# Optimization experiments

Hardware: AMD Instinct MI355X
Metric: run time of the kernel (lower is better)

## Reference

```python
import jax, jax.numpy as jnp
import numpy as np

EMBED_DIM = 256
NUM_HEADS = 8
HEAD_DIM = EMBED_DIM // NUM_HEADS
SCALE = HEAD_DIM ** -0.5  # note: scale uses head_dim even though attention is over full D
EPS = 1e-12  # torch F.normalize eps


def setup_inputs() -> dict:
    key = jax.random.key(0)
    k1, k2, k3 = jax.random.split(key, 3)
    B, Nq, Nk, D = 4, 4096, 4096, EMBED_DIM
    return {
        "query": jax.random.normal(k1, (B, Nq, D), dtype=jnp.float32),
        "key": jax.random.normal(k2, (B, Nk, D), dtype=jnp.float32),
        "value": jax.random.normal(k3, (B, Nk, D), dtype=jnp.float32),
    }


def _l2_normalize(x):
    # matches torch.nn.functional.normalize(x, dim=-1): x / max(||x||, eps)
    n = jnp.linalg.norm(x, axis=-1, keepdims=True)
    return x / jnp.maximum(n, EPS)


def reference(query, key, value):
    q = _l2_normalize(query)          # (B, Nq, D)
    k = _l2_normalize(key)            # (B, Nk, D)
    scores = jnp.einsum("bqd,bkd->bqk", q, k) * SCALE  # (B, Nq, Nk) cosine sims
    attn = jax.nn.softmax(scores, axis=-1)
    return jnp.einsum("bqk,bkd->bqd", attn, value)     # (B, Nq, D)
```

## Files before the change

### kernel.cpp

```cpp
#include <hip/hip_runtime.h>


#define NQ 4096
#define DIM 256
#define NROWS 16384
#define BM 64
#define BN 64
#define KSPLIT 4
#define NITER 16
#define PSTRIDE 68

typedef __attribute__((ext_vector_type(8))) short bf16x8;
typedef __attribute__((ext_vector_type(4))) float f32x4;
typedef __attribute__((ext_vector_type(16))) float f32x16;

__device__ __forceinline__ unsigned short f2bf(float f) {
  unsigned int u = __float_as_uint(f);
  u += 0x7fffu + ((u >> 16) & 1u);
  return (unsigned short)(u >> 16);
}

__device__ __forceinline__ float bf2f(unsigned short h) {
  return __uint_as_float((unsigned int)h << 16);
}

__device__ __forceinline__ unsigned int pack2bf(float a, float b) {
  unsigned int ua = __float_as_uint(a) + 0x8000u;
  unsigned int ub = __float_as_uint(b) + 0x8000u;
  return __builtin_amdgcn_perm(ub, ua, 0x07060302u);
}

__device__ __forceinline__ void gload16(const void* g, void* l) {
  __builtin_amdgcn_global_load_lds(
      (const __attribute__((address_space(1))) unsigned int*)g,
      (__attribute__((address_space(3))) unsigned int*)l, 16, 0, 0);
}

__global__ __launch_bounds__(256) void prep(
    const float* __restrict__ Q, const float* __restrict__ K,
    const float* __restrict__ V,
    unsigned short* __restrict__ Qrm, unsigned short* __restrict__ Kfm,
    unsigned short* __restrict__ Vfm)
{
  __shared__ unsigned short vt[64 * 264];
  const int blk = blockIdx.x, tid = threadIdx.x;
  const int wave = tid >> 6, lane = tid & 63;
  if (blk < 4096) {
    const int R = blk * 4 + wave;
    float4 v = *(const float4*)(Q + (size_t)R * DIM + lane * 4);
    float ss = v.x*v.x + v.y*v.y + v.z*v.z + v.w*v.w;
    #pragma unroll
    for (int off = 1; off < 64; off <<= 1) ss += __shfl_xor(ss, off, 64);
    float scale = (0.17677669529663687f * 1.4426950408889634f)
                  / fmaxf(sqrtf(ss), 1e-12f);
    ushort4 o;
    o.x = f2bf(v.x*scale); o.y = f2bf(v.y*scale);
    o.z = f2bf(v.z*scale); o.w = f2bf(v.w*scale);
    *(ushort4*)(Qrm + (size_t)R * DIM + lane * 4) = o;
  } else if (blk < 4352) {
    const int kt = blk - 4096;
    #pragma unroll
    for (int i = 0; i < 16; i++) {
      const int n = i*4 + wave;
      float4 v = *(const float4*)(K + ((size_t)kt*64 + n) * DIM + lane * 4);
      float ss = v.x*v.x + v.y*v.y + v.z*v.z + v.w*v.w;
      #pragma unroll
      for (int off = 1; off < 64; off <<= 1) ss += __shfl_xor(ss, off, 64);
      float scale = 1.0f / fmaxf(sqrtf(ss), 1e-12f);
      ushort4 o;
      o.x = f2bf(v.x*scale); o.y = f2bf(v.y*scale);
      o.z = f2bf(v.z*scale); o.w = f2bf(v.w*scale);
      *(ushort4*)(vt + n*264 + lane*4) = o;
    }
    __syncthreads();
    #pragma unroll
    for (int s = 0; s < 8; s++) {
      const int ch = tid + 256*s;
      const int c = ch >> 6, n = ch & 63;
      bf16x8 val = *(const bf16x8*)(vt + n*264 + c*8);
      *(bf16x8*)(Kfm + (size_t)kt*16384 + (size_t)ch*8) = val;
    }
  } else {
    const int NS = blk - 4352;
    #pragma unroll
    for (int i = 0; i < 4; i++) {
      const int e = tid + 256*i;
      const int nl = e >> 6, d = (e & 63) * 4;
      float4 v = *(const float4*)(V + ((size_t)NS*16 + nl)*DIM + d);
      ushort4 o;
      o.x = f2bf(v.x); o.y = f2bf(v.y); o.z = f2bf(v.z); o.w = f2bf(v.w);
      *(ushort4*)(vt + nl*264 + d) = o;
    }
    __syncthreads();
    #pragma unroll
    for (int i = 0; i < 2; i++) {
      const int ch = tid + 256*i;
      const int db = ch >> 6, ln = ch & 63;
      const int row0 = (ln >> 5) * 8, dd = db*32 + (ln & 31);
      ushort4 a, b;
      a.x = vt[(row0+0)*264 + dd]; a.y = vt[(row0+1)*264 + dd];
      a.z = vt[(row0+2)*264 + dd]; a.w = vt[(row0+3)*264 + dd];
      b.x = vt[(row0+4)*264 + dd]; b.y = vt[(row0+5)*264 + dd];
      b.z = vt[(row0+6)*264 + dd]; b.w = vt[(row0+7)*264 + dd];
      size_t base = ((size_t)(NS*8 + db)*64 + ln)*8;
      *(ushort4*)(Vfm + base)     = a;
      *(ushort4*)(Vfm + base + 4) = b;
    }
  }
}

__global__ __launch_bounds__(256, 4) void attn(
    const unsigned short* __restrict__ Qrm,
    const unsigned short* __restrict__ Kfm,
    const unsigned short* __restrict__ Vfm,
    unsigned short* __restrict__ Opart, float* __restrict__ lpart)
{
  __shared__ unsigned short Klds[32 * 64 * 8];
  __shared__ unsigned short Plds[BM * PSTRIDE];

  const int tid = threadIdx.x, wave = tid >> 6, lane = tid & 63;
  const int l15 = lane & 15, l4 = lane >> 4;
  const int blk = blockIdx.x;
  const int g = blk & 15, qt = blk >> 4;
  const int b = g >> 2, ks = g & 3;
  const int Rq0 = b*NQ + qt*BM;
  const int n0base = b*NQ + ks*(NQ/KSPLIT);
  const int mi = wave & 1, ni = wave >> 1;

  bf16x8 qf[2][8];
  #pragma unroll
  for (int mt = 0; mt < 2; mt++) {
    const unsigned short* qrow = Qrm + (size_t)(Rq0 + mi*32 + mt*16 + l15) * DIM + l4*8;
    #pragma unroll
    for (int kg = 0; kg < 8; kg++)
      qf[mt][kg] = *(const bf16x8*)(qrow + kg*32);
  }

  f32x16 oacc[2][2] = {};
  float lacc[2] = {};

  auto stage = [&](int kt) {
    const unsigned short* src = Kfm + (size_t)((n0base + kt*BN) >> 6) * (32*64*8);
    #pragma unroll
    for (int jj = 0; jj < 4; jj++) {
      const int c = wave*8 + jj*2;
      gload16(src + (size_t)c*512 + lane*8,     Klds + (size_t)c*512);
      gload16(src + (size_t)(c+1)*512 + lane*8, Klds + (size_t)(c+1)*512);
    }
  };

  stage(0);

  for (int kt = 0; kt < NITER; kt++) {
    __syncthreads();

    f32x4 sacc[2][2] = {};
    #pragma unroll
    for (int kg = 0; kg < 8; kg++) {
      bf16x8 kf[2];
      #pragma unroll
      for (int nt = 0; nt < 2; nt++) {
        const int nrow = ni*32 + nt*16 + l15;
        const int c = kg*4 + l4;
        kf[nt] = *(const bf16x8*)(Klds + ((size_t)(c*64 + nrow))*8);
      }
      #pragma unroll
      for (int nt = 0; nt < 2; nt++)
        #pragma unroll
        for (int mt = 0; mt < 2; mt++)
          sacc[nt][mt] = __builtin_amdgcn_mfma_f32_16x16x32_bf16(
              kf[nt], qf[mt][kg], sacc[nt][mt], 0, 0, 0);
    }

    #pragma unroll
    for (int nt = 0; nt < 2; nt++)
      #pragma unroll
      for (int mt = 0; mt < 2; mt++) {
        float p0 = __builtin_amdgcn_exp2f(sacc[nt][mt][0]);
        float p1 = __builtin_amdgcn_exp2f(sacc[nt][mt][1]);
        float p2 = __builtin_amdgcn_exp2f(sacc[nt][mt][2]);
        float p3 = __builtin_amdgcn_exp2f(sacc[nt][mt][3]);
        lacc[mt] += (p0 + p1) + (p2 + p3);
        uint2 pk;
        pk.x = pack2bf(p0, p1);
        pk.y = pack2bf(p2, p3);
        const int m = mi*32 + mt*16 + l15;
        const int n = ni*32 + nt*16 + 4*l4;
        *(uint2*)(Plds + m*PSTRIDE + n) = pk;
      }

    __syncthreads();

    if (kt + 1 < NITER) stage(kt + 1);

    const int NB0 = (n0base + kt*BN) >> 4;
    #pragma unroll
    for (int kstep = 0; kstep < 4; kstep++) {
      bf16x8 pf[2], vf[2];
      #pragma unroll
      for (int mt2 = 0; mt2 < 2; mt2++)
        pf[mt2] = *(const bf16x8*)(Plds + (mt2*32 + (lane & 31))*PSTRIDE
                                   + kstep*16 + 8*(lane >> 5));
      #pragma unroll
      for (int dt = 0; dt < 2; dt++) {
        const int db = wave*2 + dt;
        vf[dt] = *(const bf16x8*)(Vfm + ((size_t)((NB0 + kstep)*8 + db)*64 + lane)*8);
      }
      #pragma unroll
      for (int mt2 = 0; mt2 < 2; mt2++)
        #pragma unroll
        for (int dt = 0; dt < 2; dt++)
          oacc[mt2][dt] = __builtin_amdgcn_mfma_f32_32x32x16_bf16(
              pf[mt2], vf[dt], oacc[mt2][dt], 0, 0, 0);
    }
  }

  #pragma unroll
  for (int mt = 0; mt < 2; mt++) {
    float s = lacc[mt];
    s += __shfl_xor(s, 16, 64);
    s += __shfl_xor(s, 32, 64);
    if (l4 == 0)
      lpart[(size_t)(ks*2 + ni)*NROWS + Rq0 + mi*32 + mt*16 + l15] = s;
  }

  #pragma unroll
  for (int mt2 = 0; mt2 < 2; mt2++)
    #pragma unroll
    for (int dt = 0; dt < 2; dt++)
      #pragma unroll
      for (int reg = 0; reg < 16; reg++) {
        const int m = mt2*32 + 4*(lane >> 5) + (reg & 3) + 8*(reg >> 2);
        const int d = wave*64 + dt*32 + (lane & 31);
        Opart[((size_t)(ks*NROWS + Rq0 + m))*DIM + d] = f2bf(oacc[mt2][dt][reg]);
      }
}

__global__ __launch_bounds__(256) void combine(
    const unsigned short* __restrict__ Opart, const float* __restrict__ lpart,
    float* __restrict__ out)
{
  const size_t idx = (size_t)blockIdx.x*256 + threadIdx.x;
  const size_t e = idx*4;
  const int R = (int)(e >> 8);
  float acc[4] = {0.f, 0.f, 0.f, 0.f};
  #pragma unroll
  for (int s = 0; s < 4; s++) {
    ushort4 o = *(const ushort4*)(Opart + (size_t)s*NROWS*DIM + e);
    acc[0] += bf2f(o.x); acc[1] += bf2f(o.y);
    acc[2] += bf2f(o.z); acc[3] += bf2f(o.w);
  }
  float ls = 0.f;
  #pragma unroll
  for (int s = 0; s < 8; s++) ls += lpart[(size_t)s*NROWS + R];
  float inv = 1.0f / ls;
  float4 o;
  o.x = acc[0]*inv; o.y = acc[1]*inv; o.z = acc[2]*inv; o.w = acc[3]*inv;
  *(float4*)(out + e) = o;
}

extern "C" void kernel_launch(void* const* d_in, const int* in_sizes, int n_in,
                              void* d_out, int out_size, void* d_ws, size_t ws_size,
                              hipStream_t stream) {
  const float* Q = (const float*)d_in[0];
  const float* K = (const float*)d_in[1];
  const float* V = (const float*)d_in[2];
  char* ws = (char*)d_ws;
  unsigned short* Qrm  = (unsigned short*)(ws);
  unsigned short* Kfm  = (unsigned short*)(ws + 8388608);
  unsigned short* Vfm  = (unsigned short*)(ws + 16777216);
  unsigned short* Opart = (unsigned short*)(ws + 25165824);
  float* lpart = (float*)(ws + 58720256);

  prep<<<5376, 256, 0, stream>>>(Q, K, V, Qrm, Kfm, Vfm);
  attn<<<1024, 256, 0, stream>>>(Qrm, Kfm, Vfm, Opart, lpart);
  combine<<<4096, 256, 0, stream>>>(Opart, lpart, (float*)d_out);
}
```

Before: 196.3 us.

## Fuse Q normalization into attention and halve the key split

Q normalization moves out of the prep kernel and into the attention kernel, which reads fp32 Q directly, normalizes and converts it into LDS, then loads its fragments from there. This removes the Qrm round trip through global memory. The key-split factor drops from 4 to 2 with twice the iterations per block, which cuts the partial-output traffic written by attention and read by combine. Prep now handles K in 32-row halves. In exchange only 512 attention blocks launch, with launch bounds lowered to 2 blocks per CU, so the GPU may be less fully occupied. Combine still sums 4 lpart slices, which depends on how the hidden attention code writes lpart (likely 2 per split).

```diff
diff --git a/kernel.cpp b/kernel.cpp
--- a/kernel.cpp
+++ b/kernel.cpp
@@ -6,8 +6,8 @@
 #define NROWS 16384
 #define BM 64
 #define BN 64
-#define KSPLIT 4
-#define NITER 16
+#define KSPLIT 2
+#define NITER 32
 #define PSTRIDE 68
 
 typedef __attribute__((ext_vector_type(8))) short bf16x8;
@@ -37,32 +37,19 @@
 }
 
 __global__ __launch_bounds__(256) void prep(
-    const float* __restrict__ Q, const float* __restrict__ K,
-    const float* __restrict__ V,
-    unsigned short* __restrict__ Qrm, unsigned short* __restrict__ Kfm,
-    unsigned short* __restrict__ Vfm)
+    const float* __restrict__ K, const float* __restrict__ V,
+    unsigned short* __restrict__ Kfm, unsigned short* __restrict__ Vfm)
 {
-  __shared__ unsigned short vt[64 * 264];
+  __shared__ unsigned short vt[32 * 264];
   const int blk = blockIdx.x, tid = threadIdx.x;
   const int wave = tid >> 6, lane = tid & 63;
-  if (blk < 4096) {
-    const int R = blk * 4 + wave;
-    float4 v = *(const float4*)(Q + (size_t)R * DIM + lane * 4);
-    float ss = v.x*v.x + v.y*v.y + v.z*v.z + v.w*v.w;
-    #pragma unroll
-    for (int off = 1; off < 64; off <<= 1) ss += __shfl_xor(ss, off, 64);
-    float scale = (0.17677669529663687f * 1.4426950408889634f)
-                  / fmaxf(sqrtf(ss), 1e-12f);
-    ushort4 o;
-    o.x = f2bf(v.x*scale); o.y = f2bf(v.y*scale);
-    o.z = f2bf(v.z*scale); o.w = f2bf(v.w*scale);
-    *(ushort4*)(Qrm + (size_t)R * DIM + lane * 4) = o;
-  } else if (blk < 4352) {
-    const int kt = blk - 4096;
-    #pragma unroll
-    for (int i = 0; i < 16; i++) {
-      const int n = i*4 + wave;
-      float4 v = *(const float4*)(K + ((size_t)kt*64 + n) * DIM + lane * 4);
+  if (blk < 512) {
+    const int kt2 = blk;
+    const int kt = kt2 >> 1, h = kt2 & 1;
+    #pragma unroll
+    for (int i = 0; i < 8; i++) {
+      const int r = wave*8 + i;
+      float4 v = *(const float4*)(K + ((size_t)kt2*32 + r) * DIM + lane * 4);
       float ss = v.x*v.x + v.y*v.y + v.z*v.z + v.w*v.w;
       #pragma unroll
       for (int off = 1; off < 64; off <<= 1) ss += __shfl_xor(ss, off, 64);
@@ -70,18 +57,19 @@
       ushort4 o;
       o.x = f2bf(v.x*scale); o.y = f2bf(v.y*scale);
       o.z = f2bf(v.z*scale); o.w = f2bf(v.w*scale);
-      *(ushort4*)(vt + n*264 + lane*4) = o;
-    }
-    __syncthreads();
-    #pragma unroll
-    for (int s = 0; s < 8; s++) {
+      *(ushort4*)(vt + r*264 + lane*4) = o;
+    }
+    __syncthreads();
+    #pragma unroll
+    for (int s = 0; s < 4; s++) {
       const int ch = tid + 256*s;
-      const int c = ch >> 6, n = ch & 63;
-      bf16x8 val = *(const bf16x8*)(vt + n*264 + c*8);
-      *(bf16x8*)(Kfm + (size_t)kt*16384 + (size_t)ch*8) = val;
+      const int c = ch >> 5, r = ch & 31;
+      const int n = h*32 + r;
+      bf16x8 val = *(const bf16x8*)(vt + r*264 + c*8);
+      *(bf16x8*)(Kfm + (size_t)kt*16384 + (size_t)(c*64 + n)*8) = val;
     }
   } else {
-    const int NS = blk - 4352;
+    const int NS = blk - 512;
     #pragma unroll
     for (int i = 0; i < 4; i++) {
       const int e = tid + 256*i;
@@ -109,8 +97,8 @@
   }
 }
 
-__global__ __launch_bounds__(256, 4) void attn(
-    const unsigned short* __restrict__ Qrm,
+__global__ __launch_bounds__(256, 2) void attn(
+    const float* __restrict__ Qg,
     const unsigned short* __restrict__ Kfm,
     const unsigned short* __restrict__ Vfm,
     unsigned short* __restrict__ Opart, float* __restrict__ lpart)
@@ -121,20 +109,40 @@
   const int tid = threadIdx.x, wave = tid >> 6, lane = tid & 63;
   const int l15 = lane & 15, l4 = lane >> 4;
   const int blk = blockIdx.x;
-  const int g = blk & 15, qt = blk >> 4;
-  const int b = g >> 2, ks = g & 3;
+  const int g = blk & 7, qt = blk >> 3;
+  const int b = g >> 1, ks = g & 1;
   const int Rq0 = b*NQ + qt*BM;
   const int n0base = b*NQ + ks*(NQ/KSPLIT);
   const int mi = wave & 1, ni = wave >> 1;
 
+  {
+    unsigned short* Qlds = Klds;
+    #pragma unroll
+    for (int i = 0; i < 16; i++) {
+      const int r = wave*16 + i;
+      float4 v = *(const float4*)(Qg + (size_t)(Rq0 + r)*DIM + lane*4);
+      float ss = v.x*v.x + v.y*v.y + v.z*v.z + v.w*v.w;
+      #pragma unroll
+      for (int off = 1; off < 64; off <<= 1) ss += __shfl_xor(ss, off, 64);
+      float scale = (0.17677669529663687f * 1.4426950408889634f)
+                    / fmaxf(sqrtf(ss), 1e-12f);
+      ushort4 o;
+      o.x = f2bf(v.x*scale); o.y = f2bf(v.y*scale);
+      o.z = f2bf(v.z*scale); o.w = f2bf(v.w*scale);
+      *(ushort4*)(Qlds + r*DIM + lane*4) = o;
+    }
+  }
+  __syncthreads();
+
   bf16x8 qf[2][8];
   #pragma unroll
   for (int mt = 0; mt < 2; mt++) {
-    const unsigned short* qrow = Qrm + (size_t)(Rq0 + mi*32 + mt*16 + l15) * DIM + l4*8;
+    const unsigned short* qrow = Klds + (mi*32 + mt*16 + l15)*DIM + l4*8;
     #pragma unroll
     for (int kg = 0; kg < 8; kg++)
       qf[mt][kg] = *(const bf16x8*)(qrow + kg*32);
   }
+  __syncthreads();
 
   f32x16 oacc[2][2] = {};
   float lacc[2] = {};
@@ -243,19 +251,15 @@
   const size_t idx = (size_t)blockIdx.x*256 + threadIdx.x;
   const size_t e = idx*4;
   const int R = (int)(e >> 8);
-  float acc[4] = {0.f, 0.f, 0.f, 0.f};
-  #pragma unroll
-  for (int s = 0; s < 4; s++) {
-    ushort4 o = *(const ushort4*)(Opart + (size_t)s*NROWS*DIM + e);
-    acc[0] += bf2f(o.x); acc[1] += bf2f(o.y);
-    acc[2] += bf2f(o.z); acc[3] += bf2f(o.w);
-  }
-  float ls = 0.f;
-  #pragma unroll
-  for (int s = 0; s < 8; s++) ls += lpart[(size_t)s*NROWS + R];
+  ushort4 o0 = *(const ushort4*)(Opart + e);
+  ushort4 o1 = *(const ushort4*)(Opart + (size_t)NROWS*DIM + e);
+  float ls = lpart[R] + lpart[NROWS + R] + lpart[2*NROWS + R] + lpart[3*NROWS + R];
   float inv = 1.0f / ls;
   float4 o;
-  o.x = acc[0]*inv; o.y = acc[1]*inv; o.z = acc[2]*inv; o.w = acc[3]*inv;
+  o.x = (bf2f(o0.x) + bf2f(o1.x))*inv;
+  o.y = (bf2f(o0.y) + bf2f(o1.y))*inv;
+  o.z = (bf2f(o0.z) + bf2f(o1.z))*inv;
+  o.w = (bf2f(o0.w) + bf2f(o1.w))*inv;
   *(float4*)(out + e) = o;
 }
 
@@ -266,13 +270,12 @@
   const float* K = (const float*)d_in[1];
   const float* V = (const float*)d_in[2];
   char* ws = (char*)d_ws;
-  unsigned short* Qrm  = (unsigned short*)(ws);
-  unsigned short* Kfm  = (unsigned short*)(ws + 8388608);
-  unsigned short* Vfm  = (unsigned short*)(ws + 16777216);
-  unsigned short* Opart = (unsigned short*)(ws + 25165824);
-  float* lpart = (float*)(ws + 58720256);
-
-  prep<<<5376, 256, 0, stream>>>(Q, K, V, Qrm, Kfm, Vfm);
-  attn<<<1024, 256, 0, stream>>>(Qrm, Kfm, Vfm, Opart, lpart);
+  unsigned short* Kfm   = (unsigned short*)(ws);
+  unsigned short* Vfm   = (unsigned short*)(ws + 8388608);
+  unsigned short* Opart = (unsigned short*)(ws + 16777216);
+  float* lpart = (float*)(ws + 33554432);
+
+  prep<<<1536, 256, 0, stream>>>(K, V, Kfm, Vfm);
+  attn<<<512, 256, 0, stream>>>(Q, Kfm, Vfm, Opart, lpart);
   combine<<<4096, 256, 0, stream>>>(Opart, lpart, (float*)d_out);
 }
```

After: 173.5 us. 11.6% less time.

## Quantize normalized Q and K to FP8 and use FP8 MFMA for scores

Applied to the files above, without the earlier changes.

Normalized Q and K are stored as FP8 e4m3 instead of bf16, and the QK^T product uses the fp8 MFMA instruction. The softmax scale moves from the Q prep into a multiply before exp2. The prep kernel is regrouped to handle 16 Q rows per block and half K tiles, which shrinks the workspace and the K staging size in LDS. This halves Q/K bytes and doubles MFMA throughput for the score GEMM, at the cost of reduced score precision. Occupancy hint drops from 4 to 3 blocks per CU.

```diff
diff --git a/kernel.cpp b/kernel.cpp
--- a/kernel.cpp
+++ b/kernel.cpp
@@ -1,4 +1,5 @@
 #include <hip/hip_runtime.h>
+#include <hip/hip_fp8.h>
 
 
 #define NQ 4096
@@ -9,6 +10,7 @@
 #define KSPLIT 4
 #define NITER 16
 #define PSTRIDE 68
+#define SC 0.25508689738717859f
 
 typedef __attribute__((ext_vector_type(8))) short bf16x8;
 typedef __attribute__((ext_vector_type(4))) float f32x4;
@@ -24,6 +26,11 @@
   return __uint_as_float((unsigned int)h << 16);
 }
 
+__device__ __forceinline__ unsigned char f2fp8(float x) {
+  __hip_fp8_e4m3 t(x);
+  return t.__x;
+}
+
 __device__ __forceinline__ unsigned int pack2bf(float a, float b) {
   unsigned int ua = __float_as_uint(a) + 0x8000u;
   unsigned int ub = __float_as_uint(b) + 0x8000u;
@@ -39,49 +46,56 @@
 __global__ __launch_bounds__(256) void prep(
     const float* __restrict__ Q, const float* __restrict__ K,
     const float* __restrict__ V,
-    unsigned short* __restrict__ Qrm, unsigned short* __restrict__ Kfm,
+    unsigned char* __restrict__ Qf8, unsigned char* __restrict__ Kfm,
     unsigned short* __restrict__ Vfm)
 {
-  __shared__ unsigned short vt[64 * 264];
+  __shared__ unsigned short vt[32 * 264];
   const int blk = blockIdx.x, tid = threadIdx.x;
   const int wave = tid >> 6, lane = tid & 63;
-  if (blk < 4096) {
-    const int R = blk * 4 + wave;
-    float4 v = *(const float4*)(Q + (size_t)R * DIM + lane * 4);
-    float ss = v.x*v.x + v.y*v.y + v.z*v.z + v.w*v.w;
-    #pragma unroll
-    for (int off = 1; off < 64; off <<= 1) ss += __shfl_xor(ss, off, 64);
-    float scale = (0.17677669529663687f * 1.4426950408889634f)
-                  / fmaxf(sqrtf(ss), 1e-12f);
-    ushort4 o;
-    o.x = f2bf(v.x*scale); o.y = f2bf(v.y*scale);
-    o.z = f2bf(v.z*scale); o.w = f2bf(v.w*scale);
-    *(ushort4*)(Qrm + (size_t)R * DIM + lane * 4) = o;
-  } else if (blk < 4352) {
-    const int kt = blk - 4096;
-    #pragma unroll
-    for (int i = 0; i < 16; i++) {
-      const int n = i*4 + wave;
-      float4 v = *(const float4*)(K + ((size_t)kt*64 + n) * DIM + lane * 4);
+  if (blk < 1024) {
+    #pragma unroll
+    for (int i = 0; i < 4; i++) {
+      const int R = blk*16 + i*4 + wave;
+      float4 v = *(const float4*)(Q + (size_t)R * DIM + lane * 4);
       float ss = v.x*v.x + v.y*v.y + v.z*v.z + v.w*v.w;
       #pragma unroll
       for (int off = 1; off < 64; off <<= 1) ss += __shfl_xor(ss, off, 64);
-      float scale = 1.0f / fmaxf(sqrtf(ss), 1e-12f);
-      ushort4 o;
-      o.x = f2bf(v.x*scale); o.y = f2bf(v.y*scale);
-      o.z = f2bf(v.z*scale); o.w = f2bf(v.w*scale);
-      *(ushort4*)(vt + n*264 + lane*4) = o;
-    }
-    __syncthreads();
-    #pragma unroll
-    for (int s = 0; s < 8; s++) {
+      float s = 1.0f / fmaxf(sqrtf(ss), 1e-12f);
+      unsigned int pk = (unsigned int)f2fp8(v.x*s)
+                      | ((unsigned int)f2fp8(v.y*s) << 8)
+                      | ((unsigned int)f2fp8(v.z*s) << 16)
+                      | ((unsigned int)f2fp8(v.w*s) << 24);
+      *(unsigned int*)(Qf8 + (size_t)R * DIM + lane * 4) = pk;
+    }
+  } else if (blk < 1536) {
+    const int kt2 = blk - 1024;
+    unsigned char* vtb = (unsigned char*)vt;
+    #pragma unroll
+    for (int i = 0; i < 8; i++) {
+      const int r = wave*8 + i;
+      float4 v = *(const float4*)(K + ((size_t)kt2*32 + r) * DIM + lane * 4);
+      float ss = v.x*v.x + v.y*v.y + v.z*v.z + v.w*v.w;
+      #pragma unroll
+      for (int off = 1; off < 64; off <<= 1) ss += __shfl_xor(ss, off, 64);
+      float s = 1.0f / fmaxf(sqrtf(ss), 1e-12f);
+      unsigned int pk = (unsigned int)f2fp8(v.x*s)
+                      | ((unsigned int)f2fp8(v.y*s) << 8)
+                      | ((unsigned int)f2fp8(v.z*s) << 16)
+                      | ((unsigned int)f2fp8(v.w*s) << 24);
+      *(unsigned int*)(vtb + r*264 + lane*4) = pk;
+    }
+    __syncthreads();
+    const int kt = kt2 >> 1, h = kt2 & 1;
+    #pragma unroll
+    for (int s = 0; s < 4; s++) {
       const int ch = tid + 256*s;
-      const int c = ch >> 6, n = ch & 63;
-      bf16x8 val = *(const bf16x8*)(vt + n*264 + c*8);
-      *(bf16x8*)(Kfm + (size_t)kt*16384 + (size_t)ch*8) = val;
+      const int c = ch >> 5, r = ch & 31;
+      const int n = h*32 + r;
+      long val = *(const long*)(vtb + r*264 + c*8);
+      *(long*)(Kfm + (size_t)kt*16384 + (size_t)(c*64 + n)*8) = val;
     }
   } else {
-    const int NS = blk - 4352;
+    const int NS = blk - 1536;
     #pragma unroll
     for (int i = 0; i < 4; i++) {
       const int e = tid + 256*i;
@@ -109,13 +123,13 @@
   }
 }
 
-__global__ __launch_bounds__(256, 4) void attn(
-    const unsigned short* __restrict__ Qrm,
-    const unsigned short* __restrict__ Kfm,
+__global__ __launch_bounds__(256, 3) void attn(
+    const unsigned char* __restrict__ Qf8,
+    const unsigned char* __restrict__ Kfm,
     const unsigned short* __restrict__ Vfm,
     unsigned short* __restrict__ Opart, float* __restrict__ lpart)
 {
-  __shared__ unsigned short Klds[32 * 64 * 8];
+  __shared__ unsigned char Klds[16384];
   __shared__ unsigned short Plds[BM * PSTRIDE];
 
   const int tid = threadIdx.x, wave = tid >> 6, lane = tid & 63;
@@ -127,25 +141,24 @@
   const int n0base = b*NQ + ks*(NQ/KSPLIT);
   const int mi = wave & 1, ni = wave >> 1;
 
-  bf16x8 qf[2][8];
+  long qf[2][8];
   #pragma unroll
   for (int mt = 0; mt < 2; mt++) {
-    const unsigned short* qrow = Qrm + (size_t)(Rq0 + mi*32 + mt*16 + l15) * DIM + l4*8;
+    const unsigned char* qrow = Qf8 + (size_t)(Rq0 + mi*32 + mt*16 + l15)*DIM + l4*8;
     #pragma unroll
     for (int kg = 0; kg < 8; kg++)
-      qf[mt][kg] = *(const bf16x8*)(qrow + kg*32);
+      qf[mt][kg] = *(const long*)(qrow + kg*32);
   }
 
   f32x16 oacc[2][2] = {};
   float lacc[2] = {};
 
   auto stage = [&](int kt) {
-    const unsigned short* src = Kfm + (size_t)((n0base + kt*BN) >> 6) * (32*64*8);
+    const unsigned char* src = Kfm + (size_t)((n0base + kt*BN) >> 6) * 16384;
     #pragma unroll
     for (int jj = 0; jj < 4; jj++) {
-      const int c = wave*8 + jj*2;
-      gload16(src + (size_t)c*512 + lane*8,     Klds + (size_t)c*512);
-      gload16(src + (size_t)(c+1)*512 + lane*8, Klds + (size_t)(c+1)*512);
+      const int off = wave*4096 + jj*1024 + lane*16;
+      gload16(src + off, Klds + off);
     }
   };
 
@@ -157,18 +170,17 @@
     f32x4 sacc[2][2] = {};
     #pragma unroll
     for (int kg = 0; kg < 8; kg++) {
-      bf16x8 kf[2];
+      long kf[2];
       #pragma unroll
       for (int nt = 0; nt < 2; nt++) {
         const int nrow = ni*32 + nt*16 + l15;
-        const int c = kg*4 + l4;
-        kf[nt] = *(const bf16x8*)(Klds + ((size_t)(c*64 + nrow))*8);
+        kf[nt] = *(const long*)(Klds + (kg*4 + l4)*512 + nrow*8);
       }
       #pragma unroll
       for (int nt = 0; nt < 2; nt++)
         #pragma unroll
         for (int mt = 0; mt < 2; mt++)
-          sacc[nt][mt] = __builtin_amdgcn_mfma_f32_16x16x32_bf16(
+          sacc[nt][mt] = __builtin_amdgcn_mfma_f32_16x16x32_fp8_fp8(
               kf[nt], qf[mt][kg], sacc[nt][mt], 0, 0, 0);
     }
 
@@ -176,10 +188,10 @@
     for (int nt = 0; nt < 2; nt++)
       #pragma unroll
       for (int mt = 0; mt < 2; mt++) {
-        float p0 = __builtin_amdgcn_exp2f(sacc[nt][mt][0]);
-        float p1 = __builtin_amdgcn_exp2f(sacc[nt][mt][1]);
-        float p2 = __builtin_amdgcn_exp2f(sacc[nt][mt][2]);
-        float p3 = __builtin_amdgcn_exp2f(sacc[nt][mt][3]);
+        float p0 = __builtin_amdgcn_exp2f(sacc[nt][mt][0] * SC);
+        float p1 = __builtin_amdgcn_exp2f(sacc[nt][mt][1] * SC);
+        float p2 = __builtin_amdgcn_exp2f(sacc[nt][mt][2] * SC);
+        float p3 = __builtin_amdgcn_exp2f(sacc[nt][mt][3] * SC);
         lacc[mt] += (p0 + p1) + (p2 + p3);
         uint2 pk;
         pk.x = pack2bf(p0, p1);
@@ -266,13 +278,13 @@
   const float* K = (const float*)d_in[1];
   const float* V = (const float*)d_in[2];
   char* ws = (char*)d_ws;
-  unsigned short* Qrm  = (unsigned short*)(ws);
-  unsigned short* Kfm  = (unsigned short*)(ws + 8388608);
-  unsigned short* Vfm  = (unsigned short*)(ws + 16777216);
-  unsigned short* Opart = (unsigned short*)(ws + 25165824);
-  float* lpart = (float*)(ws + 58720256);
-
-  prep<<<5376, 256, 0, stream>>>(Q, K, V, Qrm, Kfm, Vfm);
-  attn<<<1024, 256, 0, stream>>>(Qrm, Kfm, Vfm, Opart, lpart);
+  unsigned char*  Qf8   = (unsigned char*)(ws);
+  unsigned char*  Kfm   = (unsigned char*)(ws + 4194304);
+  unsigned short* Vfm   = (unsigned short*)(ws + 8388608);
+  unsigned short* Opart = (unsigned short*)(ws + 16777216);
+  float* lpart = (float*)(ws + 50331648);
+
+  prep<<<2560, 256, 0, stream>>>(Q, K, V, Qf8, Kfm, Vfm);
+  attn<<<1024, 256, 0, stream>>>(Qf8, Kfm, Vfm, Opart, lpart);
   combine<<<4096, 256, 0, stream>>>(Opart, lpart, (float*)d_out);
 }
```

After: 175.6 us. -10.5%, faster.
